# Performance work log

Hardware: AMD Instinct MI355X
Metric: run time of the kernel (lower is better)

Reference implementation:

```python
import jax, jax.numpy as jnp
import numpy as np

SM_SCALE = 0.08838834764831845  # 1/sqrt(128)
SLIDING_WINDOW = 128
N_TOKENS, N_HEADS, Q_MULT, D_HEAD = 2048, 8, 4, 128


def setup_inputs() -> dict:
    key = jax.random.key(0)
    k1, k2, k3, k4 = jax.random.split(key, 4)
    Q = jax.random.normal(k1, (N_TOKENS, N_HEADS, Q_MULT, D_HEAD), dtype=jnp.float32)
    K = jax.random.normal(k2, (N_TOKENS, N_HEADS, D_HEAD), dtype=jnp.float32)
    V = jax.random.normal(k3, (N_TOKENS, N_HEADS, D_HEAD), dtype=jnp.float32)
    S = jax.random.normal(k4, (N_HEADS * Q_MULT,), dtype=jnp.float32)
    return {"Q": Q, "K": K, "V": V, "S": S}


def _build_mask(n_tokens, sliding_window, dtype):
    q_idx = jnp.arange(n_tokens)[:, None]
    k_idx = jnp.arange(n_tokens)[None, :]
    # causal: disallow k > q; sliding window: disallow k <= q - sliding_window
    disallowed = k_idx > q_idx
    if sliding_window > 0:
        disallowed = disallowed | (k_idx <= q_idx - sliding_window)
    return jnp.where(disallowed, jnp.array(-jnp.inf, dtype), jnp.array(0.0, dtype))


def reference(Q, K, V, S):
    n_tokens, n_heads, q_mult, d_head = Q.shape
    mask = _build_mask(n_tokens, SLIDING_WINDOW, Q.dtype)  # (T, T)
    # scores: (h, m, q, k)
    QK = jnp.einsum('qhmd,khd->hmqk', Q, K) * SM_SCALE
    QK = QK + mask[None, None, :, :]
    # append per-(head, q_mult) sink logit as an extra key column
    sink = jnp.broadcast_to(S.reshape(n_heads, q_mult, 1, 1),
                            (n_heads, q_mult, n_tokens, 1))
    QK = jnp.concatenate([QK, sink], axis=-1)  # (h, m, q, k+1)
    W = jax.nn.softmax(QK, axis=-1)[..., :-1]  # drop sink column
    attn = jnp.einsum('hmqk,khd->qhmd', W, V)
    return attn.reshape(n_tokens, n_heads * q_mult * d_head)
```

## Files before the change

### kernel.cpp

```cpp
#include <hip/hip_runtime.h>
#include <cstdint>

#define T_TOK 2048
#define NH 8
#define QM 4
#define DH 128
#define BQ 64
#define ROWS 256
#define CK 32
#define KS 136
#define VS 40
#define PS 40
#define SM_SCALE 0.08838834764831845f

typedef __attribute__((ext_vector_type(8))) short short8v;
typedef __attribute__((ext_vector_type(4))) short short4v;
typedef __attribute__((ext_vector_type(2))) short short2v;
typedef __attribute__((ext_vector_type(4))) float floatx4;

static __device__ __forceinline__ short f2bf(float x) {
  union { float f; unsigned u; } v; v.f = x;
  return (short)((v.u + 0x7fffu + ((v.u >> 16) & 1u)) >> 16);
}

__global__ __launch_bounds__(1024, 4)
void attn_fwd(const float* __restrict__ Qp, const float* __restrict__ Kp,
              const float* __restrict__ Vp, const float* __restrict__ Sp,
              float* __restrict__ Op) {
  __shared__ short k_s[2][CK * KS];
  __shared__ short v_s[2][DH * VS];
  __shared__ short p_s[ROWS * PS];

  const int t    = threadIdx.x;
  const int lane = t & 63;
  const int wv   = t >> 6;
  const int quad = lane >> 4;
  const int l16  = lane & 15;

  const int bx = blockIdx.x;
  const int h  = bx & 7;
  const int q0 = (bx >> 3) * BQ;
  const int lo0 = q0 > 127 ? q0 - 127 : 0;
  const int nk  = q0 + BQ - lo0;
  const int nch = (nk + CK - 1) >> 5;

  const int Ra = wv * 16 + l16;
  const int qa = q0 + (Ra >> 2), ma = Ra & 3;
  const float* qptr = Qp + ((size_t)qa * (NH * QM) + h * QM + ma) * DH + quad * 8;
  short8v qf[4];
#pragma unroll
  for (int s = 0; s < 4; ++s) {
    float4 x0 = *(const float4*)(qptr + 32 * s);
    float4 x1 = *(const float4*)(qptr + 32 * s + 4);
    short8v f;
    f[0] = f2bf(x0.x); f[1] = f2bf(x0.y); f[2] = f2bf(x0.z); f[3] = f2bf(x0.w);
    f[4] = f2bf(x1.x); f[5] = f2bf(x1.y); f[6] = f2bf(x1.z); f[7] = f2bf(x1.w);
    qf[s] = f;
  }

  const int kj  = t >> 5;
  const int kd4 = (t & 31) * 4;
  const int vd  = t & 127;
  const int vg  = t >> 7;

  const int qc = q0 + wv * 4 + quad;
  float dn[4] = {0.f, 0.f, 0.f, 0.f};
  floatx4 oacc[8];
#pragma unroll
  for (int nt = 0; nt < 8; ++nt) oacc[nt] = (floatx4)0.0f;

  float4 pk;
  float  pv[4];
  {
    int g = lo0 + kj; g = g < T_TOK ? g : T_TOK - 1;
    pk = *(const float4*)(Kp + ((size_t)g * NH + h) * DH + kd4);
#pragma unroll
    for (int u = 0; u < 4; ++u) {
      const int s = vg * 4 + u;
      int gk = lo0 + (s >> 1) + ((s & 1) << 4);
      gk = gk < T_TOK ? gk : T_TOK - 1;
      pv[u] = Vp[((size_t)gk * NH + h) * DH + vd];
    }
  }

  for (int c = 0; c < nch; ++c) {
    const int b  = c & 1;
    const int kb = lo0 + c * CK;

    {
      short4v s4;
      s4[0] = f2bf(pk.x); s4[1] = f2bf(pk.y); s4[2] = f2bf(pk.z); s4[3] = f2bf(pk.w);
      *(short4v*)(&k_s[b][kj * KS + kd4]) = s4;
      short4v t4;
      t4[0] = f2bf(pv[0]); t4[1] = f2bf(pv[1]); t4[2] = f2bf(pv[2]); t4[3] = f2bf(pv[3]);
      *(short4v*)(&v_s[b][vd * VS + vg * 4]) = t4;
    }
    __syncthreads();

    if (c + 1 < nch) {
      const int kb2 = kb + CK;
      int g = kb2 + kj; g = g < T_TOK ? g : T_TOK - 1;
      pk = *(const float4*)(Kp + ((size_t)g * NH + h) * DH + kd4);
#pragma unroll
      for (int u = 0; u < 4; ++u) {
        const int s = vg * 4 + u;
        int gk = kb2 + (s >> 1) + ((s & 1) << 4);
        gk = gk < T_TOK ? gk : T_TOK - 1;
        pv[u] = Vp[((size_t)gk * NH + h) * DH + vd];
      }
    }

    floatx4 sc0 = (floatx4)0.0f, sc1 = (floatx4)0.0f;
#pragma unroll
    for (int s = 0; s < 4; ++s) {
      short8v k0 = *(const short8v*)(&k_s[b][l16 * KS + quad * 8 + 32 * s]);
      short8v k1 = *(const short8v*)(&k_s[b][(l16 + 16) * KS + quad * 8 + 32 * s]);
      sc0 = __builtin_amdgcn_mfma_f32_16x16x32_bf16(qf[s], k0, sc0, 0, 0, 0);
      sc1 = __builtin_amdgcn_mfma_f32_16x16x32_bf16(qf[s], k1, sc1, 0, 0, 0);
    }

    const int k0i = kb + l16, k1i = kb + 16 + l16;
    const bool ok0 = (k0i <= qc) && (k0i > qc - 128);
    const bool ok1 = (k1i <= qc) && (k1i > qc - 128);
#pragma unroll
    for (int r = 0; r < 4; ++r) {
      float e0 = ok0 ? __expf(sc0[r] * SM_SCALE) : 0.f;
      float e1 = ok1 ? __expf(sc1[r] * SM_SCALE) : 0.f;
      dn[r] += e0 + e1;
      const int R = wv * 16 + quad * 4 + r;
      short2v p2; p2[0] = f2bf(e0); p2[1] = f2bf(e1);
      *(short2v*)(&p_s[R * PS + 2 * l16]) = p2;
    }

    short8v pf = *(const short8v*)(&p_s[(wv * 16 + l16) * PS + quad * 8]);
#pragma unroll
    for (int nt = 0; nt < 8; ++nt) {
      short8v vf = *(const short8v*)(&v_s[b][(l16 + 16 * nt) * VS + quad * 8]);
      oacc[nt] = __builtin_amdgcn_mfma_f32_16x16x32_bf16(pf, vf, oacc[nt], 0, 0, 0);
    }
  }

#pragma unroll
  for (int r = 0; r < 4; ++r) {
    float s = dn[r];
#pragma unroll
    for (int mm = 1; mm <= 8; mm <<= 1) s += __shfl_xor(s, mm);
    const float total = s + __expf(Sp[h * QM + r]);
    const float rd = 1.0f / total;
    float* ob = Op + (size_t)qc * (NH * QM * DH) + ((size_t)h * QM + r) * DH + l16;
#pragma unroll
    for (int nt = 0; nt < 8; ++nt) ob[nt * 16] = oacc[nt][r] * rd;
  }
}

extern "C" void kernel_launch(void* const* d_in, const int* in_sizes, int n_in,
                              void* d_out, int out_size, void* d_ws, size_t ws_size,
                              hipStream_t stream) {
  const float* Q = (const float*)d_in[0];
  const float* K = (const float*)d_in[1];
  const float* V = (const float*)d_in[2];
  const float* S = (const float*)d_in[3];
  float* O = (float*)d_out;
  const int grid = (T_TOK / BQ) * NH;
  attn_fwd<<<dim3(grid), dim3(1024), 0, stream>>>(Q, K, V, S, O);
}
```

Measured before the change: 103.6 us.

## Shrink query tile to 16 tokens with 256-thread blocks and wider staging loads

Reduces the query block from 64 to 16 tokens per workgroup and the block size from 1024 to 256 threads, giving four times as many workgroups. Each thread now stages 16 K elements and 16 V elements per chunk with 8-wide LDS stores. The aim is more parallelism and a smaller per-block key range, with less redundant key work inside each sliding window. The cost is that overlapping K/V windows are reloaded from global memory by more blocks, and each thread holds more registers for the prefetched data.

```diff
diff --git a/kernel.cpp b/kernel.cpp
--- a/kernel.cpp
+++ b/kernel.cpp
@@ -5,8 +5,8 @@
 #define NH 8
 #define QM 4
 #define DH 128
-#define BQ 64
-#define ROWS 256
+#define BQ 16
+#define ROWS 64
 #define CK 32
 #define KS 136
 #define VS 40
@@ -14,7 +14,6 @@
 #define SM_SCALE 0.08838834764831845f
 
 typedef __attribute__((ext_vector_type(8))) short short8v;
-typedef __attribute__((ext_vector_type(4))) short short4v;
 typedef __attribute__((ext_vector_type(2))) short short2v;
 typedef __attribute__((ext_vector_type(4))) float floatx4;
 
@@ -23,7 +22,7 @@
   return (short)((v.u + 0x7fffu + ((v.u >> 16) & 1u)) >> 16);
 }
 
-__global__ __launch_bounds__(1024, 4)
+__global__ __launch_bounds__(256, 3)
 void attn_fwd(const float* __restrict__ Qp, const float* __restrict__ Kp,
               const float* __restrict__ Vp, const float* __restrict__ Sp,
               float* __restrict__ Op) {
@@ -58,10 +57,10 @@
     qf[s] = f;
   }
 
-  const int kj  = t >> 5;
-  const int kd4 = (t & 31) * 4;
-  const int vd  = t & 127;
-  const int vg  = t >> 7;
+  const int kj   = t >> 3;
+  const int kd16 = (t & 7) * 16;
+  const int vd   = t & 127;
+  const int vg   = t >> 7;
 
   const int qc = q0 + wv * 4 + quad;
   float dn[4] = {0.f, 0.f, 0.f, 0.f};
@@ -69,14 +68,16 @@
 #pragma unroll
   for (int nt = 0; nt < 8; ++nt) oacc[nt] = (floatx4)0.0f;
 
-  float4 pk;
-  float  pv[4];
+  float4 pk[4];
+  float  pv[16];
   {
     int g = lo0 + kj; g = g < T_TOK ? g : T_TOK - 1;
-    pk = *(const float4*)(Kp + ((size_t)g * NH + h) * DH + kd4);
+    const float* kp = Kp + ((size_t)g * NH + h) * DH + kd16;
 #pragma unroll
-    for (int u = 0; u < 4; ++u) {
-      const int s = vg * 4 + u;
+    for (int w = 0; w < 4; ++w) pk[w] = *(const float4*)(kp + 4 * w);
+#pragma unroll
+    for (int u = 0; u < 16; ++u) {
+      const int s = vg * 16 + u;
       int gk = lo0 + (s >> 1) + ((s & 1) << 4);
       gk = gk < T_TOK ? gk : T_TOK - 1;
       pv[u] = Vp[((size_t)gk * NH + h) * DH + vd];
@@ -88,22 +89,31 @@
     const int kb = lo0 + c * CK;
 
     {
-      short4v s4;
-      s4[0] = f2bf(pk.x); s4[1] = f2bf(pk.y); s4[2] = f2bf(pk.z); s4[3] = f2bf(pk.w);
-      *(short4v*)(&k_s[b][kj * KS + kd4]) = s4;
-      short4v t4;
-      t4[0] = f2bf(pv[0]); t4[1] = f2bf(pv[1]); t4[2] = f2bf(pv[2]); t4[3] = f2bf(pv[3]);
-      *(short4v*)(&v_s[b][vd * VS + vg * 4]) = t4;
+      short8v a8, b8;
+#pragma unroll
+      for (int u = 0; u < 4; ++u) {
+        a8[u]     = f2bf(pk[0][u]); a8[u + 4] = f2bf(pk[1][u]);
+        b8[u]     = f2bf(pk[2][u]); b8[u + 4] = f2bf(pk[3][u]);
+      }
+      *(short8v*)(&k_s[b][kj * KS + kd16])     = a8;
+      *(short8v*)(&k_s[b][kj * KS + kd16 + 8]) = b8;
+      short8v t8a, t8b;
+#pragma unroll
+      for (int u = 0; u < 8; ++u) { t8a[u] = f2bf(pv[u]); t8b[u] = f2bf(pv[u + 8]); }
+      *(short8v*)(&v_s[b][vd * VS + vg * 16])     = t8a;
+      *(short8v*)(&v_s[b][vd * VS + vg * 16 + 8]) = t8b;
     }
     __syncthreads();
 
     if (c + 1 < nch) {
       const int kb2 = kb + CK;
       int g = kb2 + kj; g = g < T_TOK ? g : T_TOK - 1;
-      pk = *(const float4*)(Kp + ((size_t)g * NH + h) * DH + kd4);
+      const float* kp = Kp + ((size_t)g * NH + h) * DH + kd16;
 #pragma unroll
-      for (int u = 0; u < 4; ++u) {
-        const int s = vg * 4 + u;
+      for (int w = 0; w < 4; ++w) pk[w] = *(const float4*)(kp + 4 * w);
+#pragma unroll
+      for (int u = 0; u < 16; ++u) {
+        const int s = vg * 16 + u;
         int gk = kb2 + (s >> 1) + ((s & 1) << 4);
         gk = gk < T_TOK ? gk : T_TOK - 1;
         pv[u] = Vp[((size_t)gk * NH + h) * DH + vd];
@@ -162,5 +172,5 @@
   const float* S = (const float*)d_in[3];
   float* O = (float*)d_out;
   const int grid = (T_TOK / BQ) * NH;
-  attn_fwd<<<dim3(grid), dim3(1024), 0, stream>>>(Q, K, V, S, O);
+  attn_fwd<<<dim3(grid), dim3(256), 0, stream>>>(Q, K, V, S, O);
 }
```

Result: slower. 110.5 us (+6.6%).
